# Kernel optimization log

Hardware: AMD Instinct MI355X
Metric: run time of the kernel (lower is better)

The kernel has to match this reference:

```python
import jax, jax.numpy as jnp
import numpy as np

DIM = 1024
HEADS = 16
HEAD_DIM = DIM // HEADS
HIDDEN = 4 * DIM
EPS = 1e-5


def layer_norm(x, g, b):
    mu = jnp.mean(x, axis=-1, keepdims=True)
    var = jnp.var(x, axis=-1, keepdims=True)
    return (x - mu) * jax.lax.rsqrt(var + EPS) * g + b


def setup_inputs() -> dict:
    key = jax.random.key(0)
    ks = jax.random.split(key, 8)
    B, N, C = 2, 2048, DIM
    # xavier-uniform-ish scales
    s_qkv = float(np.sqrt(6.0 / (C + 3 * C)))
    s_proj = float(np.sqrt(6.0 / (C + C)))
    s_fc1 = float(np.sqrt(6.0 / (C + HIDDEN)))
    return {
        "x": jax.random.normal(ks[0], (B, N, C), jnp.float32),
        "w_qkv": jax.random.uniform(ks[1], (3 * C, C), jnp.float32, -s_qkv, s_qkv),
        "w_proj": jax.random.uniform(ks[2], (C, C), jnp.float32, -s_proj, s_proj),
        "b_proj": jnp.zeros((C,), jnp.float32),
        "ln1_g": jnp.ones((C,), jnp.float32),
        "ln1_b": jnp.zeros((C,), jnp.float32),
        "ln2_g": jnp.ones((C,), jnp.float32),
        "ln2_b": jnp.zeros((C,), jnp.float32),
        "w_fc1": jax.random.uniform(ks[3], (HIDDEN, C), jnp.float32, -s_fc1, s_fc1),
        "b_fc1": jnp.zeros((HIDDEN,), jnp.float32),
        "w_fc2": jax.random.uniform(ks[4], (C, HIDDEN), jnp.float32, -s_fc1, s_fc1),
        "b_fc2": jnp.zeros((C,), jnp.float32),
    }


def attention(x, w_qkv, w_proj, b_proj):
    B, N, C = x.shape
    qkv = x @ w_qkv.T  # [B,N,3C]
    qkv = qkv.reshape(B, N, 3, HEADS, HEAD_DIM).transpose(2, 0, 3, 1, 4)
    q, k, v = qkv[0], qkv[1], qkv[2]  # [B,H,N,hd]
    scale = HEAD_DIM ** -0.5
    attn = jnp.einsum("bhqd,bhkd->bhqk", q, k) * scale
    attn = jax.nn.softmax(attn, axis=-1)
    out = jnp.einsum("bhqk,bhkd->bhqd", attn, v)  # [B,H,N,hd]
    out = out.transpose(0, 2, 1, 3).reshape(B, N, C)
    return out @ w_proj.T + b_proj


def reference(x, w_qkv, w_proj, b_proj, ln1_g, ln1_b, ln2_g, ln2_b, w_fc1, b_fc1, w_fc2, b_fc2):
    x = x + attention(layer_norm(x, ln1_g, ln1_b), w_qkv, w_proj, b_proj)
    h = layer_norm(x, ln2_g, ln2_b)
    h = jax.nn.gelu(h @ w_fc1.T + b_fc1, approximate=False)
    x = x + (h @ w_fc2.T + b_fc2)
    return x
```

## Files before the change

kernel.cpp:

```cpp
#include <hip/hip_runtime.h>
#include <hip/hip_bf16.h>
#include <math.h>

typedef __bf16 bf16;
typedef __attribute__((ext_vector_type(8))) __bf16 bf16x8;
typedef __attribute__((ext_vector_type(4))) __bf16 bf16x4;
typedef __attribute__((ext_vector_type(4))) float f32x4;

#define DEV static __device__ __forceinline__

typedef const void __attribute__((address_space(1)))* gptr_t;
typedef void __attribute__((address_space(3)))* lptr_t;

DEV void async16(const void* g, void* l) {
  __builtin_amdgcn_global_load_lds((gptr_t)g, (lptr_t)l, 16, 0, 0);
}

DEV void wg_barrier() {
  __builtin_amdgcn_sched_barrier(0);
  __builtin_amdgcn_s_barrier();
  __builtin_amdgcn_sched_barrier(0);
}

__global__ __launch_bounds__(256) void f2b4_kernel(const float* __restrict__ s0,
                                                   const float* __restrict__ s1,
                                                   const float* __restrict__ s2,
                                                   const float* __restrict__ s3,
                                                   bf16* __restrict__ d0, bf16* __restrict__ d1,
                                                   bf16* __restrict__ d2, bf16* __restrict__ d3,
                                                   int n0, int n1, int n2, int n3) {
  int i = (blockIdx.x * 256 + threadIdx.x) * 4;
  const float* s;
  bf16* d;
  int off;
  if (i < n0) { s = s0; d = d0; off = i; }
  else if (i < n0 + n1) { s = s1; d = d1; off = i - n0; }
  else if (i < n0 + n1 + n2) { s = s2; d = d2; off = i - n0 - n1; }
  else if (i < n0 + n1 + n2 + n3) { s = s3; d = d3; off = i - n0 - n1 - n2; }
  else return;
  float4 v = *(const float4*)(s + off);
  d[off + 0] = (bf16)v.x;
  d[off + 1] = (bf16)v.y;
  d[off + 2] = (bf16)v.z;
  d[off + 3] = (bf16)v.w;
}

__global__ __launch_bounds__(256) void ln_kernel(const float* __restrict__ in,
                                                 const float* __restrict__ g,
                                                 const float* __restrict__ b,
                                                 bf16* __restrict__ out) {
  const int row = blockIdx.x;
  const int tid = threadIdx.x;
  float4 v = ((const float4*)(in + (size_t)row * 1024))[tid];
  float s = v.x + v.y + v.z + v.w;
  float s2 = v.x * v.x + v.y * v.y + v.z * v.z + v.w * v.w;
#pragma unroll
  for (int off = 1; off < 64; off <<= 1) {
    s += __shfl_xor(s, off);
    s2 += __shfl_xor(s2, off);
  }
  __shared__ float red[8];
  int w = tid >> 6, lane = tid & 63;
  if (lane == 0) { red[w] = s; red[4 + w] = s2; }
  __syncthreads();
  s = red[0] + red[1] + red[2] + red[3];
  s2 = red[4] + red[5] + red[6] + red[7];
  const float mean = s * (1.f / 1024.f);
  const float var = s2 * (1.f / 1024.f) - mean * mean;
  const float rstd = rsqrtf(var + 1e-5f);
  float4 gv = ((const float4*)g)[tid];
  float4 bv = ((const float4*)b)[tid];
  bf16* orow = out + (size_t)row * 1024 + tid * 4;
  orow[0] = (bf16)((v.x - mean) * rstd * gv.x + bv.x);
  orow[1] = (bf16)((v.y - mean) * rstd * gv.y + bv.y);
  orow[2] = (bf16)((v.z - mean) * rstd * gv.z + bv.z);
  orow[3] = (bf16)((v.w - mean) * rstd * gv.w + bv.w);
}

template <int EPI>
__global__ __launch_bounds__(512, 2) void gemm256(const bf16* __restrict__ A,
                                                  const bf16* __restrict__ B,
                                                  bf16* __restrict__ outb,
                                                  const float* __restrict__ bias,
                                                  int M, int N, int K, int gridN) {
  __shared__ bf16 As[2][256 * 64];
  __shared__ bf16 Bs[2][256 * 64];
  const int nwg = gridDim.x;
  const int bid = blockIdx.x;
  const int swz = (bid & 7) * (nwg >> 3) + (bid >> 3);
  const int bx = swz % gridN, by = swz / gridN;
  const int brow = by * 256, bcol = bx * 256;
  const int tid = threadIdx.x;
  const int lane = tid & 63, wid = tid >> 6;
  const int wm = wid >> 2, wn = wid & 3;
  const int lr = lane & 15, lk4 = lane >> 4;
  const int strow = tid >> 3, stc = tid & 7;
  const int NT = K >> 6;
  f32x4 acc[8][4] = {};

#define STAGE(tt, bb)                                                                   \
  {                                                                                     \
    const int k0_ = (tt)*64;                                                            \
    _Pragma("unroll") for (int s_ = 0; s_ < 4; ++s_) {                                  \
      const int r_ = s_ * 64 + strow;                                                   \
      const int g_ = (stc ^ (strow & 7)) * 8;                                           \
      async16(A + (size_t)(brow + r_) * K + k0_ + g_, &As[bb][r_ * 64 + stc * 8]);      \
      async16(B + (size_t)(bcol + r_) * K + k0_ + g_, &Bs[bb][r_ * 64 + stc * 8]);      \
    }                                                                                   \
  }

  STAGE(0, 0);
  STAGE(1, 1);
  asm volatile("s_waitcnt vmcnt(8)" ::: "memory");
  wg_barrier();

  for (int t = 0; t < NT; ++t) {
    const int cur = t & 1;
    bf16x8 af[8][2], bfr[4][2];
#pragma unroll
    for (int m = 0; m < 8; ++m)
#pragma unroll
      for (int kk = 0; kk < 2; ++kk) {
        const int row = wm * 128 + m * 16 + lr;
        const int kc = kk * 4 + lk4;
        af[m][kk] = *(const bf16x8*)&As[cur][row * 64 + ((kc ^ (row & 7)) * 8)];
      }
#pragma unroll
    for (int n = 0; n < 4; ++n)
#pragma unroll
      for (int kk = 0; kk < 2; ++kk) {
        const int row = wn * 64 + n * 16 + lr;
        const int kc = kk * 4 + lk4;
        bfr[n][kk] = *(const bf16x8*)&Bs[cur][row * 64 + ((kc ^ (row & 7)) * 8)];
      }
    asm volatile("s_waitcnt lgkmcnt(0)" ::: "memory");
    wg_barrier();
    if (t + 2 < NT) STAGE(t + 2, cur);
    __builtin_amdgcn_s_setprio(1);
#pragma unroll
    for (int m = 0; m < 8; ++m)
#pragma unroll
      for (int n = 0; n < 4; ++n) {
        acc[m][n] = __builtin_amdgcn_mfma_f32_16x16x32_bf16(af[m][0], bfr[n][0], acc[m][n], 0, 0, 0);
        acc[m][n] = __builtin_amdgcn_mfma_f32_16x16x32_bf16(af[m][1], bfr[n][1], acc[m][n], 0, 0, 0);
      }
    __builtin_amdgcn_s_setprio(0);
    if (t + 1 < NT) {
      if (t + 2 < NT) {
        asm volatile("s_waitcnt vmcnt(8)" ::: "memory");
      } else {
        asm volatile("s_waitcnt vmcnt(0)" ::: "memory");
      }
      wg_barrier();
    }
  }
#undef STAGE
  const int r0 = brow + wm * 128 + lk4 * 4;
  const int c0 = bcol + wn * 64 + lr;
  float bias_v[4];
  if (EPI == 1) {
#pragma unroll
    for (int n = 0; n < 4; ++n) bias_v[n] = bias[c0 + n * 16];
  }
#pragma unroll
  for (int m = 0; m < 8; ++m)
#pragma unroll
    for (int n = 0; n < 4; ++n)
#pragma unroll
      for (int j = 0; j < 4; ++j) {
        const int r = r0 + m * 16 + j;
        const int c = c0 + n * 16;
        float v = acc[m][n][j];
        if (EPI == 1) {
          v += bias_v[n];
          v = 0.5f * v * (1.0f + erff(v * 0.70710678118654752f));
        }
        outb[(size_t)r * N + c] = (bf16)v;
      }
}

__global__ __launch_bounds__(512, 2) void gemm128(const bf16* __restrict__ A,
                                                  const bf16* __restrict__ B,
                                                  float* __restrict__ outf,
                                                  const float* __restrict__ bias,
                                                  const float* __restrict__ resid,
                                                  int M, int N, int K, int gridN) {
  __shared__ bf16 As[2][128 * 64];
  __shared__ bf16 Bs[2][128 * 64];
  const int nwg = gridDim.x;
  const int bid = blockIdx.x;
  const int swz = (bid & 7) * (nwg >> 3) + (bid >> 3);
  const int bx = swz % gridN, by = swz / gridN;
  const int brow = by * 128, bcol = bx * 128;
  const int tid = threadIdx.x;
  const int lane = tid & 63, wid = tid >> 6;
  const int wm = wid >> 2, wn = wid & 3;
  const int lr = lane & 15, lk4 = lane >> 4;
  const int strow = tid >> 3, stc = tid & 7;
  const int NT = K >> 6;
  f32x4 acc[4][2] = {};

#define STAGE1(tt, bb)                                                                  \
  {                                                                                     \
    const int k0_ = (tt)*64;                                                            \
    _Pragma("unroll") for (int s_ = 0; s_ < 2; ++s_) {                                  \
      const int r_ = s_ * 64 + strow;                                                   \
      const int g_ = (stc ^ (strow & 7)) * 8;                                           \
      async16(A + (size_t)(brow + r_) * K + k0_ + g_, &As[bb][r_ * 64 + stc * 8]);      \
      async16(B + (size_t)(bcol + r_) * K + k0_ + g_, &Bs[bb][r_ * 64 + stc * 8]);      \
    }                                                                                   \
  }

  STAGE1(0, 0);
  STAGE1(1, 1);
  asm volatile("s_waitcnt vmcnt(4)" ::: "memory");
  wg_barrier();

  for (int t = 0; t < NT; ++t) {
    const int cur = t & 1;
    bf16x8 af[4][2], bfr[2][2];
#pragma unroll
    for (int m = 0; m < 4; ++m)
#pragma unroll
      for (int kk = 0; kk < 2; ++kk) {
        const int row = wm * 64 + m * 16 + lr;
        const int kc = kk * 4 + lk4;
        af[m][kk] = *(const bf16x8*)&As[cur][row * 64 + ((kc ^ (row & 7)) * 8)];
      }
#pragma unroll
    for (int n = 0; n < 2; ++n)
#pragma unroll
      for (int kk = 0; kk < 2; ++kk) {
        const int row = wn * 32 + n * 16 + lr;
        const int kc = kk * 4 + lk4;
        bfr[n][kk] = *(const bf16x8*)&Bs[cur][row * 64 + ((kc ^ (row & 7)) * 8)];
      }
    asm volatile("s_waitcnt lgkmcnt(0)" ::: "memory");
    wg_barrier();
    if (t + 2 < NT) STAGE1(t + 2, cur);
    __builtin_amdgcn_s_setprio(1);
#pragma unroll
    for (int m = 0; m < 4; ++m)
#pragma unroll
      for (int n = 0; n < 2; ++n) {
        acc[m][n] = __builtin_amdgcn_mfma_f32_16x16x32_bf16(af[m][0], bfr[n][0], acc[m][n], 0, 0, 0);
        acc[m][n] = __builtin_amdgcn_mfma_f32_16x16x32_bf16(af[m][1], bfr[n][1], acc[m][n], 0, 0, 0);
      }
    __builtin_amdgcn_s_setprio(0);
    if (t + 1 < NT) {
      if (t + 2 < NT) {
        asm volatile("s_waitcnt vmcnt(4)" ::: "memory");
      } else {
        asm volatile("s_waitcnt vmcnt(0)" ::: "memory");
      }
      wg_barrier();
    }
  }
#undef STAGE1
  const int r0 = brow + wm * 64 + lk4 * 4;
  const int c0 = bcol + wn * 32 + lr;
#pragma unroll
  for (int m = 0; m < 4; ++m)
#pragma unroll
    for (int n = 0; n < 2; ++n)
#pragma unroll
      for (int j = 0; j < 4; ++j) {
        const int r = r0 + m * 16 + j;
        const int c = c0 + n * 16;
        outf[(size_t)r * N + c] = acc[m][n][j] + bias[c] + resid[(size_t)r * N + c];
      }
}

__global__ __launch_bounds__(512, 4) void flash_kernel(const bf16* __restrict__ qkv,
                                                       bf16* __restrict__ out) {
  const int bid = blockIdx.x;
  const int swz = (bid & 7) * 64 + (bid >> 3);
  const int qt = swz & 15;
  const int bh = swz >> 4;
  const int b = bh >> 4, h = bh & 15;
  const int tid = threadIdx.x;
  const int lane = tid & 63, w = tid >> 6;
  const int lr = lane & 15, lk4 = lane >> 4;
  const bf16* Qp = qkv + (size_t)(b * 2048) * 3072 + h * 64;
  const bf16* Kp = Qp + 1024;
  const bf16* Vp = Qp + 2048;
  __shared__ bf16 Ks[2][64 * 64];
  __shared__ bf16 VTs[2][64 * 64];
  __shared__ bf16 Ps[128 * 64 + 4096];
  const int qw0 = qt * 128 + w * 16;
  const float SC = 0.125f * 1.44269504f;
  const float THRU = 8.0f / SC;
  bf16x8 qf[2];
#pragma unroll
  for (int kk = 0; kk < 2; ++kk)
    qf[kk] = *(const bf16x8*)(Qp + (size_t)(qw0 + lr) * 3072 + kk * 32 + lk4 * 8);
  f32x4 o[4] = {};
  float mrun = -1e30f, lrun = 0.f;
  const int sr = tid >> 3, sc8 = tid & 7;
  const int vd = tid & 63, vkc = (tid >> 6) * 8;
  const int vch = tid >> 6;
  const int prow = (w * 16 + lr) * 64;
  bf16 vv[8];
  async16(Kp + (size_t)sr * 3072 + (sc8 ^ (sr & 7)) * 8, &Ks[0][sr * 64 + sc8 * 8]);
#pragma unroll
  for (int j = 0; j < 8; ++j) vv[j] = Vp[(size_t)(vkc + j) * 3072 + vd];
  {
    bf16x8 a;
#pragma unroll
    for (int j = 0; j < 8; ++j) a[j] = vv[j];
    *(bf16x8*)&VTs[0][vd * 64 + ((vch ^ (vd & 7)) * 8)] = a;
  }
  __syncthreads();
  for (int t = 0; t < 32; ++t) {
    const int cur = t & 1, nxt = cur ^ 1;
    if (t < 31) {
      const size_t kv0n = (size_t)(t + 1) * 64;
      async16(Kp + (kv0n + sr) * 3072 + (sc8 ^ (sr & 7)) * 8, &Ks[nxt][sr * 64 + sc8 * 8]);
#pragma unroll
      for (int j = 0; j < 8; ++j) vv[j] = Vp[(kv0n + vkc + j) * 3072 + vd];
    }
    f32x4 st[4] = {};
    __builtin_amdgcn_s_setprio(1);
#pragma unroll
    for (int n = 0; n < 4; ++n)
#pragma unroll
      for (int kk = 0; kk < 2; ++kk) {
        bf16x8 kf = *(const bf16x8*)&Ks[cur][(n * 16 + lr) * 64 + (((kk * 4 + lk4) ^ (lr & 7)) * 8)];
        st[n] = __builtin_amdgcn_mfma_f32_16x16x32_bf16(kf, qf[kk], st[n], 0, 0, 0);
      }
    __builtin_amdgcn_s_setprio(0);
    float m01 = fmaxf(fmaxf(st[0][0], st[0][1]), fmaxf(st[0][2], st[0][3]));
    float m23 = fmaxf(fmaxf(st[1][0], st[1][1]), fmaxf(st[1][2], st[1][3]));
    float m45 = fmaxf(fmaxf(st[2][0], st[2][1]), fmaxf(st[2][2], st[2][3]));
    float m67 = fmaxf(fmaxf(st[3][0], st[3][1]), fmaxf(st[3][2], st[3][3]));
    float mx = fmaxf(fmaxf(m01, m23), fmaxf(m45, m67));
    mx = fmaxf(mx, __shfl_xor(mx, 16));
    mx = fmaxf(mx, __shfl_xor(mx, 32));
    const bool skip = __all(mx <= mrun + THRU);
    const float mn = skip ? mrun : fmaxf(mrun, mx);
    const float mnS = mn * SC;
    float rs = 0.f;
#pragma unroll
    for (int n = 0; n < 4; ++n) {
      float p0 = exp2f(fmaf(st[n][0], SC, -mnS));
      float p1 = exp2f(fmaf(st[n][1], SC, -mnS));
      float p2 = exp2f(fmaf(st[n][2], SC, -mnS));
      float p3 = exp2f(fmaf(st[n][3], SC, -mnS));
      rs += (p0 + p1) + (p2 + p3);
      bf16x4 pk;
      pk[0] = (bf16)p0; pk[1] = (bf16)p1; pk[2] = (bf16)p2; pk[3] = (bf16)p3;
      *(bf16x4*)&Ps[prow + (((n * 2 + (lk4 >> 1)) ^ (lr & 7)) * 8) + (lk4 & 1) * 4] = pk;
    }
    rs += __shfl_xor(rs, 16);
    rs += __shfl_xor(rs, 32);
    if (!skip) {
      const float alpha = exp2f(fmaf(mrun, SC, -mnS));
      lrun = lrun * alpha + rs;
      mrun = mn;
#pragma unroll
      for (int c = 0; c < 4; ++c)
#pragma unroll
        for (int j = 0; j < 4; ++j) o[c][j] *= alpha;
    } else {
      lrun += rs;
    }
    bf16x8 pb[2];
#pragma unroll
    for (int kk = 0; kk < 2; ++kk)
      pb[kk] = *(const bf16x8*)&Ps[prow + (((kk * 4 + lk4) ^ (lr & 7)) * 8)];
    __builtin_amdgcn_s_setprio(1);
#pragma unroll
    for (int c = 0; c < 4; ++c)
#pragma unroll
      for (int kk = 0; kk < 2; ++kk) {
        bf16x8 vfr = *(const bf16x8*)&VTs[cur][(c * 16 + lr) * 64 + (((kk * 4 + lk4) ^ (lr & 7)) * 8)];
        o[c] = __builtin_amdgcn_mfma_f32_16x16x32_bf16(vfr, pb[kk], o[c], 0, 0, 0);
      }
    __builtin_amdgcn_s_setprio(0);
    if (t < 31) {
      bf16x8 a;
#pragma unroll
      for (int j = 0; j < 8; ++j) a[j] = vv[j];
      *(bf16x8*)&VTs[nxt][vd * 64 + ((vch ^ (vd & 7)) * 8)] = a;
    }
    __syncthreads();
  }
  const float inv = 1.f / lrun;
#pragma unroll
  for (int c = 0; c < 4; ++c) {
    bf16x4 ov;
#pragma unroll
    for (int j = 0; j < 4; ++j) ov[j] = (bf16)(o[c][j] * inv);
    *(bf16x4*)&out[(size_t)(b * 2048 + qw0 + lr) * 1024 + h * 64 + c * 16 + lk4 * 4] = ov;
  }
}

extern "C" void kernel_launch(void* const* d_in, const int* in_sizes, int n_in,
                              void* d_out, int out_size, void* d_ws, size_t ws_size,
                              hipStream_t stream) {
  const float* x      = (const float*)d_in[0];
  const float* w_qkv  = (const float*)d_in[1];
  const float* w_proj = (const float*)d_in[2];
  const float* b_proj = (const float*)d_in[3];
  const float* ln1_g  = (const float*)d_in[4];
  const float* ln1_b  = (const float*)d_in[5];
  const float* ln2_g  = (const float*)d_in[6];
  const float* ln2_b  = (const float*)d_in[7];
  const float* w_fc1  = (const float*)d_in[8];
  const float* b_fc1  = (const float*)d_in[9];
  const float* w_fc2  = (const float*)d_in[10];
  const float* b_fc2  = (const float*)d_in[11];

  char* W = (char*)d_ws;
  bf16* wqkvb = (bf16*)(W + 0);
  bf16* wprojb = (bf16*)(W + 6291456);
  bf16* wfc1b = (bf16*)(W + 8388608);
  bf16* wfc2b = (bf16*)(W + 16777216);
  bf16* xn    = (bf16*)(W + 25165824);
  bf16* qkvb  = (bf16*)(W + 33554432);
  bf16* attnb = (bf16*)(W + 58720256);
  float* x2   = (float*)(W + 67108864);
  bf16* hbuf  = (bf16*)(W + 83886080);
  float* outf = (float*)d_out;

  f2b4_kernel<<<12288, 256, 0, stream>>>(w_qkv, w_proj, w_fc1, w_fc2,
                                         wqkvb, wprojb, wfc1b, wfc2b,
                                         3145728, 1048576, 4194304, 4194304);

  ln_kernel<<<4096, 256, 0, stream>>>(x, ln1_g, ln1_b, xn);
  gemm256<0><<<192, 512, 0, stream>>>(xn, wqkvb, qkvb, nullptr, 4096, 3072, 1024, 12);
  flash_kernel<<<512, 512, 0, stream>>>(qkvb, attnb);
  gemm128<<<256, 512, 0, stream>>>(attnb, wprojb, x2, b_proj, x, 4096, 1024, 1024, 8);
  ln_kernel<<<4096, 256, 0, stream>>>(x2, ln2_g, ln2_b, xn);
  gemm256<1><<<256, 512, 0, stream>>>(xn, wfc1b, hbuf, b_fc1, 4096, 4096, 1024, 16);
  gemm128<<<256, 512, 0, stream>>>(hbuf, wfc2b, outf, b_fc2, x2, 4096, 1024, 4096, 8);
}
```

Before: 251.1 us.

## Split K across warp pairs in gemm128 with LDS reduction of accumulators

Warps in gemm128 now form a 2x2x2 layout. Each warp computes a 64x64 output sub-tile over half of every 64-wide K slice, where it previously covered a 64x32 sub-tile over the full slice. Each MFMA now reuses more A and B fragments from LDS, so fewer fragment loads are needed per MFMA. The cost is doubled accumulator registers and an extra epilogue step: the wk=1 warps write partial sums to LDS, and after a barrier the wk=0 warps add them in before applying bias and residual. The higher register use may hurt occupancy under the (512,2) launch bound.

```diff
diff --git a/kernel.cpp b/kernel.cpp
--- a/kernel.cpp
+++ b/kernel.cpp
@@ -194,11 +194,11 @@
   const int brow = by * 128, bcol = bx * 128;
   const int tid = threadIdx.x;
   const int lane = tid & 63, wid = tid >> 6;
-  const int wm = wid >> 2, wn = wid & 3;
+  const int wk = wid & 1, wn = (wid >> 1) & 1, wm = wid >> 2;
   const int lr = lane & 15, lk4 = lane >> 4;
   const int strow = tid >> 3, stc = tid & 7;
   const int NT = K >> 6;
-  f32x4 acc[4][2] = {};
+  f32x4 acc[4][4] = {};
 
 #define STAGE1(tt, bb)                                                                  \
   {                                                                                     \
@@ -216,25 +216,20 @@
   asm volatile("s_waitcnt vmcnt(4)" ::: "memory");
   wg_barrier();
 
+  const int kc = wk * 4 + lk4;
   for (int t = 0; t < NT; ++t) {
     const int cur = t & 1;
-    bf16x8 af[4][2], bfr[2][2];
-#pragma unroll
-    for (int m = 0; m < 4; ++m)
-#pragma unroll
-      for (int kk = 0; kk < 2; ++kk) {
-        const int row = wm * 64 + m * 16 + lr;
-        const int kc = kk * 4 + lk4;
-        af[m][kk] = *(const bf16x8*)&As[cur][row * 64 + ((kc ^ (row & 7)) * 8)];
-      }
-#pragma unroll
-    for (int n = 0; n < 2; ++n)
-#pragma unroll
-      for (int kk = 0; kk < 2; ++kk) {
-        const int row = wn * 32 + n * 16 + lr;
-        const int kc = kk * 4 + lk4;
-        bfr[n][kk] = *(const bf16x8*)&Bs[cur][row * 64 + ((kc ^ (row & 7)) * 8)];
-      }
+    bf16x8 af[4], bfr[4];
+#pragma unroll
+    for (int m = 0; m < 4; ++m) {
+      const int row = wm * 64 + m * 16 + lr;
+      af[m] = *(const bf16x8*)&As[cur][row * 64 + ((kc ^ (row & 7)) * 8)];
+    }
+#pragma unroll
+    for (int n = 0; n < 4; ++n) {
+      const int row = wn * 64 + n * 16 + lr;
+      bfr[n] = *(const bf16x8*)&Bs[cur][row * 64 + ((kc ^ (row & 7)) * 8)];
+    }
     asm volatile("s_waitcnt lgkmcnt(0)" ::: "memory");
     wg_barrier();
     if (t + 2 < NT) STAGE1(t + 2, cur);
@@ -242,10 +237,8 @@
 #pragma unroll
     for (int m = 0; m < 4; ++m)
 #pragma unroll
-      for (int n = 0; n < 2; ++n) {
-        acc[m][n] = __builtin_amdgcn_mfma_f32_16x16x32_bf16(af[m][0], bfr[n][0], acc[m][n], 0, 0, 0);
-        acc[m][n] = __builtin_amdgcn_mfma_f32_16x16x32_bf16(af[m][1], bfr[n][1], acc[m][n], 0, 0, 0);
-      }
+      for (int n = 0; n < 4; ++n)
+        acc[m][n] = __builtin_amdgcn_mfma_f32_16x16x32_bf16(af[m], bfr[n], acc[m][n], 0, 0, 0);
     __builtin_amdgcn_s_setprio(0);
     if (t + 1 < NT) {
       if (t + 2 < NT) {
@@ -257,18 +250,39 @@
     }
   }
 #undef STAGE1
-  const int r0 = brow + wm * 64 + lk4 * 4;
-  const int c0 = bcol + wn * 32 + lr;
-#pragma unroll
-  for (int m = 0; m < 4; ++m)
-#pragma unroll
-    for (int n = 0; n < 2; ++n)
-#pragma unroll
-      for (int j = 0; j < 4; ++j) {
-        const int r = r0 + m * 16 + j;
-        const int c = c0 + n * 16;
-        outf[(size_t)r * N + c] = acc[m][n][j] + bias[c] + resid[(size_t)r * N + c];
-      }
+  __syncthreads();
+  {
+    const int r = wm * 2 + wn;
+    float* reg = (r < 2) ? ((float*)&As[0][0] + r * 4096)
+                         : ((float*)&Bs[0][0] + (r - 2) * 4096);
+    if (wk == 1) {
+#pragma unroll
+      for (int m = 0; m < 4; ++m)
+#pragma unroll
+        for (int n = 0; n < 4; ++n)
+#pragma unroll
+          for (int j = 0; j < 4; ++j)
+            reg[(m * 16 + n * 4 + j) * 64 + lane] = acc[m][n][j];
+    }
+    __syncthreads();
+    if (wk == 0) {
+      const int r0 = brow + wm * 64 + lk4 * 4;
+      const int c0 = bcol + wn * 64 + lr;
+#pragma unroll
+      for (int m = 0; m < 4; ++m)
+#pragma unroll
+        for (int n = 0; n < 4; ++n) {
+          const int c = c0 + n * 16;
+          const float bv = bias[c];
+#pragma unroll
+          for (int j = 0; j < 4; ++j) {
+            const int rr = r0 + m * 16 + j;
+            float v = acc[m][n][j] + reg[(m * 16 + n * 4 + j) * 64 + lane];
+            outf[(size_t)rr * N + c] = v + bv + resid[(size_t)rr * N + c];
+          }
+        }
+    }
+  }
 }
 
 __global__ __launch_bounds__(512, 4) void flash_kernel(const bf16* __restrict__ qkv,
```

New measurement: 250.6 us. About the same (-0.2%).
